# Kernel optimization log

Measured on AMD Instinct MI355X. Metric: run time of the kernel, lower is better.

The kernel has to match this reference:

```python
import jax, jax.numpy as jnp
import numpy as np

# module config
D = 1024      # d_model
H = 16        # n_heads
DK = D // H   # head dim (rotary dim)
HI = 4        # indexer heads
DI = 64       # indexer dim
K = 512       # layer_top_k (adaptive_k fixed to layer default)
B, S = 2, 2048


def setup_inputs() -> dict:
    key = jax.random.key(0)
    ks = jax.random.split(key, 6)
    sc = 0.02
    return {
        "x": jax.random.normal(ks[0], (B, S, D), jnp.float32),
        "w_qkv": jax.random.normal(ks[1], (3 * D, D), jnp.float32) * sc,
        "w_o": jax.random.normal(ks[2], (D, D), jnp.float32) * sc,
        "w_qi": jax.random.normal(ks[3], (HI * DI, D), jnp.float32) * sc,
        "w_ki": jax.random.normal(ks[4], (DI, D), jnp.float32) * sc,
        "w_wi": jax.random.normal(ks[5], (HI, D), jnp.float32) * sc,
    }


def _rope(x):
    # torchtune-style interleaved RoPE; x: [b, s, h, d]
    d = x.shape[-1]
    s = x.shape[1]
    inv = 1.0 / (10000.0 ** (jnp.arange(0, d, 2, dtype=jnp.float32) / d))
    ang = jnp.arange(s, dtype=jnp.float32)[:, None] * inv  # [s, d/2]
    cos = jnp.cos(ang)[None, :, None, :]
    sin = jnp.sin(ang)[None, :, None, :]
    x1, x2 = x[..., ::2], x[..., 1::2]
    return jnp.stack([x1 * cos - x2 * sin, x1 * sin + x2 * cos], axis=-1).reshape(x.shape)


def reference(x, w_qkv, w_o, w_qi, w_ki, w_wi):
    b, s, _ = x.shape
    # QKV projection -> [b, s, 3, H, DK]
    qkv = (x @ w_qkv.T).reshape(b, s, 3, H, DK)
    q, k, v = qkv[:, :, 0], qkv[:, :, 1], qkv[:, :, 2]  # [b, s, h, dk]
    q = _rope(q)
    k = _rope(k)

    # Lightning indexer: I[t,s] = sum_j w[t,j] * relu(q_idx[t,j] . k_idx[s])
    qi = (x @ w_qi.T).reshape(b, s, HI, DI)
    ki = x @ w_ki.T            # [b, s, DI]
    wi = x @ w_wi.T            # [b, s, HI]
    dots = jnp.einsum('bthd,bsd->bths', qi, ki)
    idx_scores = (jax.nn.relu(dots) * wi[:, :, :, None]).sum(axis=2)  # [b, t, s]

    # causal mask then top-k selection -> boolean allow-mask via scatter
    causal = jnp.triu(jnp.ones((s, s), dtype=bool), 1)
    masked_scores = jnp.where(causal[None], -jnp.inf, idx_scores)
    _, top_idx = jax.lax.top_k(masked_scores, K)  # [b, t, K]
    allow = jnp.zeros((b, s, s), dtype=bool).at[
        jnp.arange(b)[:, None, None], jnp.arange(s)[None, :, None], top_idx
    ].set(True)

    # gated sparse attention: SDPA with additive mask (0 where selected, -inf else)
    scores = jnp.einsum('bthd,bshd->bhts', q, k) / jnp.sqrt(jnp.float32(DK))
    scores = jnp.where(allow[:, None], scores, -jnp.inf)
    attn = jax.nn.softmax(scores, axis=-1)
    out = jnp.einsum('bhts,bshd->bthd', attn, v).reshape(b, s, D)
    return out @ w_o.T
```

## Files before the change

### kernel.cpp

```cpp
#include <hip/hip_runtime.h>
#include <hip/hip_bf16.h>
#include <math.h>

namespace {

constexpr int cB = 2, cS = 2048, cD = 1024, cH = 16, cHI = 4, cDI = 64, cK = 512;
constexpr int cNT = cB * cS;
constexpr int QKV_STRIDE = 3 * cD;

typedef __bf16 bf16x8 __attribute__((ext_vector_type(8)));
typedef float f32x4 __attribute__((ext_vector_type(4)));

__device__ __forceinline__ unsigned packbf2(float a, float b)
{
    __hip_bfloat16 ba = __float2bfloat16(a), bb = __float2bfloat16(b);
    return (unsigned)*(unsigned short*)&ba | ((unsigned)*(unsigned short*)&bb << 16);
}

__global__ void pack_bf16(const float* __restrict__ src, __hip_bfloat16* __restrict__ dst, int n)
{
    int i = blockIdx.x * 256 + threadIdx.x;
    if (i < n) dst[i] = __float2bfloat16(src[i]);
}

__global__ __launch_bounds__(256) void mfma_gemm_bt(const __hip_bfloat16* __restrict__ A,
                                                    const __hip_bfloat16* __restrict__ B,
                                                    float* __restrict__ C, int M, int N, int K)
{
    __shared__ unsigned short Als[128][40];
    __shared__ unsigned short Bls[128][40];
    const int tid = threadIdx.x;
    const int m0 = blockIdx.y * 128, n0 = blockIdx.x * 128;
    const int w = tid >> 6, lane = tid & 63;
    const int mw = (w >> 1) * 64, nw = (w & 1) * 64;
    const int lr = lane & 15, quad = lane >> 4;
    const unsigned short* Au = (const unsigned short*)A;
    const unsigned short* Bu = (const unsigned short*)B;
    f32x4 acc[4][4] = {};
    for (int k0 = 0; k0 < K; k0 += 32) {
#pragma unroll
        for (int i = 0; i < 2; i++) {
            int c = tid + i * 256;
            int row = c >> 2, kc = c & 3;
            uint4 av = *(const uint4*)(Au + (size_t)(m0 + row) * K + k0 + kc * 8);
            uint4 bv = *(const uint4*)(Bu + (size_t)(n0 + row) * K + k0 + kc * 8);
            *(uint4*)&Als[row][kc * 8] = av;
            *(uint4*)&Bls[row][kc * 8] = bv;
        }
        __syncthreads();
        bf16x8 af[4], bfr[4];
#pragma unroll
        for (int i = 0; i < 4; i++) af[i] = *(const bf16x8*)&Als[mw + i * 16 + lr][quad * 8];
#pragma unroll
        for (int j = 0; j < 4; j++) bfr[j] = *(const bf16x8*)&Bls[nw + j * 16 + lr][quad * 8];
#pragma unroll
        for (int i = 0; i < 4; i++)
#pragma unroll
            for (int j = 0; j < 4; j++)
                acc[i][j] = __builtin_amdgcn_mfma_f32_16x16x32_bf16(af[i], bfr[j], acc[i][j], 0, 0, 0);
        __syncthreads();
    }
#pragma unroll
    for (int i = 0; i < 4; i++)
#pragma unroll
        for (int j = 0; j < 4; j++)
#pragma unroll
            for (int r = 0; r < 4; r++) {
                int m = m0 + mw + i * 16 + quad * 4 + r;
                int n = n0 + nw + j * 16 + lr;
                C[(size_t)m * N + n] = acc[i][j][r];
            }
}

__global__ void gemm_idx(const float* __restrict__ A, const float* __restrict__ w_qi,
                         const float* __restrict__ w_ki, const float* __restrict__ w_wi,
                         float* __restrict__ qi, float* __restrict__ ki, float* __restrict__ wi)
{
    __shared__ float As[32][68];
    __shared__ float Bs[32][68];
    const int tid = threadIdx.x;
    const int m0 = blockIdx.y * 64, n0 = blockIdx.x * 64;
    const int ty = tid >> 4, tx = tid & 15;
    float acc[4][4] = {};
    for (int k0 = 0; k0 < cD; k0 += 32) {
#pragma unroll
        for (int i = 0; i < 8; i++) {
            int idx = tid + i * 256;
            int r = idx >> 5, kk = idx & 31;
            As[kk][r] = A[(size_t)(m0 + r) * cD + k0 + kk];
            const int nr = n0 + r;
            float bv = 0.f;
            if (nr < 256) bv = w_qi[(size_t)nr * cD + k0 + kk];
            else if (nr < 320) bv = w_ki[(size_t)(nr - 256) * cD + k0 + kk];
            else if (nr < 324) bv = w_wi[(size_t)(nr - 320) * cD + k0 + kk];
            Bs[kk][r] = bv;
        }
        __syncthreads();
#pragma unroll
        for (int kk = 0; kk < 32; kk++) {
            float a[4], b[4];
#pragma unroll
            for (int i = 0; i < 4; i++) a[i] = As[kk][ty * 4 + i];
#pragma unroll
            for (int j = 0; j < 4; j++) b[j] = Bs[kk][tx * 4 + j];
#pragma unroll
            for (int i = 0; i < 4; i++)
#pragma unroll
                for (int j = 0; j < 4; j++) acc[i][j] = fmaf(a[i], b[j], acc[i][j]);
        }
        __syncthreads();
    }
#pragma unroll
    for (int i = 0; i < 4; i++) {
        int m = m0 + ty * 4 + i;
#pragma unroll
        for (int j = 0; j < 4; j++) {
            int n = n0 + tx * 4 + j;
            if (n < 256) qi[(size_t)m * 256 + n] = acc[i][j];
            else if (n < 320) ki[(size_t)m * 64 + (n - 256)] = acc[i][j];
            else if (n < 324) wi[(size_t)m * 4 + (n - 320)] = acc[i][j];
        }
    }
}

__global__ void rope_pack(const float* __restrict__ qkv, __hip_bfloat16* __restrict__ qkvb)
{
    const int idx = blockIdx.x * 256 + threadIdx.x;
    const int c = idx & 511, tok = idx >> 9;
    const int i = c & 31;
    const int s = tok & (cS - 1);
    const float inv = powf(10000.f, -(float)(2 * i) / 64.f);
    float sn, cs;
    sincosf((float)s * inv, &sn, &cs);
    const size_t base = (size_t)tok * QKV_STRIDE + (c >> 5) * 64 + 2 * i;
    unsigned* dst = (unsigned*)qkvb;
    float x1 = qkv[base], x2 = qkv[base + 1];
    dst[base >> 1] = packbf2(x1 * cs - x2 * sn, x1 * sn + x2 * cs);
    x1 = qkv[base + cD]; x2 = qkv[base + cD + 1];
    dst[(base + cD) >> 1] = packbf2(x1 * cs - x2 * sn, x1 * sn + x2 * cs);
    dst[(base + 2 * cD) >> 1] = packbf2(qkv[base + 2 * cD], qkv[base + 2 * cD + 1]);
}

__global__ __launch_bounds__(256) void indexer_scores(const float* __restrict__ qi,
                                                      const float* __restrict__ ki,
                                                      const float* __restrict__ wi,
                                                      float* __restrict__ scores)
{
    const int b = blockIdx.z;
    const int t0 = blockIdx.y * 128, s0 = blockIdx.x * 64;
    if (s0 > t0 + 127) return;
    __shared__ float Qs[128][68];
    __shared__ float Ks[64][68];
    const int tid = threadIdx.x;
    const int ty = tid >> 4, tx = tid & 15;
#pragma unroll
    for (int i = 0; i < 4; i++) {
        int c = tid + i * 256;
        int r = c >> 4, cq = c & 15;
        *(float4*)&Ks[r][cq * 4] = *(const float4*)&ki[((size_t)(b * cS + s0 + r)) * cDI + cq * 4];
    }
    float acc[8][4] = {};
    for (int h = 0; h < cHI; h++) {
        __syncthreads();
#pragma unroll
        for (int i = 0; i < 8; i++) {
            int c = tid + i * 256;
            int r = c >> 4, cq = c & 15;
            *(float4*)&Qs[r][cq * 4] =
                *(const float4*)&qi[((size_t)(b * cS + t0 + r)) * (cHI * cDI) + h * cDI + cq * 4];
        }
        __syncthreads();
        float w8[8];
#pragma unroll
        for (int i = 0; i < 8; i++) w8[i] = wi[((size_t)(b * cS + t0 + ty + i * 16)) * cHI + h];
        float dot[8][4] = {};
        for (int d = 0; d < 64; d += 4) {
            float4 a4[8], b4[4];
#pragma unroll
            for (int i = 0; i < 8; i++) a4[i] = *(const float4*)&Qs[ty + i * 16][d];
#pragma unroll
            for (int j = 0; j < 4; j++) b4[j] = *(const float4*)&Ks[tx + j * 16][d];
#pragma unroll
            for (int i = 0; i < 8; i++)
#pragma unroll
                for (int j = 0; j < 4; j++) {
                    dot[i][j] = fmaf(a4[i].x, b4[j].x, dot[i][j]);
                    dot[i][j] = fmaf(a4[i].y, b4[j].y, dot[i][j]);
                    dot[i][j] = fmaf(a4[i].z, b4[j].z, dot[i][j]);
                    dot[i][j] = fmaf(a4[i].w, b4[j].w, dot[i][j]);
                }
        }
#pragma unroll
        for (int i = 0; i < 8; i++)
#pragma unroll
            for (int j = 0; j < 4; j++) acc[i][j] += fmaxf(dot[i][j], 0.f) * w8[i];
    }
#pragma unroll
    for (int i = 0; i < 8; i++) {
        int t = t0 + ty + i * 16;
#pragma unroll
        for (int j = 0; j < 4; j++) {
            int s = s0 + tx + j * 16;
            if (s <= t) scores[((size_t)(b * cS) + t) * cS + s] = acc[i][j];
        }
    }
}

__device__ __forceinline__ unsigned mapf(float f)
{
    unsigned u = __float_as_uint(f);
    if (u == 0x80000000u) u = 0u;
    return (u & 0x80000000u) ? ~u : (u | 0x80000000u);
}

__global__ void topk_select(const float* __restrict__ scores, unsigned* __restrict__ allow_w)
{
    const int row = blockIdx.x;
    const int t = row & (cS - 1);
    const int tid = threadIdx.x;
    unsigned* aw = allow_w + (size_t)row * 64;
    if (t < cK) {
        if (tid < 64) aw[tid] = (tid < 16) ? 0xFFFFFFFFu : 0u;
        return;
    }
    const float* sr = scores + (size_t)row * cS;
    const int n = t + 1;
    __shared__ unsigned ukeys[cS];
    __shared__ int whist[4][16];
    __shared__ unsigned abits[64];
    __shared__ int wsum[4];
    __shared__ unsigned sh_prefix;
    __shared__ int sh_rem, sh_eqbase;
    for (int s = tid; s < n; s += 256) ukeys[s] = mapf(sr[s]);
    if (tid < 64) abits[tid] = 0u;
    if (tid == 0) { sh_prefix = 0u; sh_rem = cK; }
    __syncthreads();
    const int wl = tid >> 6, ln = tid & 63;
    for (int pass = 0; pass < 8; pass++) {
        const int shift = 28 - 4 * pass;
        const unsigned prefix = sh_prefix;
        const unsigned himask = pass ? (0xFFFFFFFFu << (shift + 4)) : 0u;
        unsigned cnt = 0;
        for (int sb = wl * 64; sb < n; sb += 256) {
            const int s = sb + ln;
            const bool active = (s < n) && ((ukeys[s] & himask) == prefix);
            const unsigned digit = active ? ((ukeys[s] >> shift) & 15u) : 0xFFu;
#pragma unroll
            for (int bin = 0; bin < 16; bin++) {
                const unsigned long long bal = __ballot(active && (digit == (unsigned)bin));
                if (ln == bin) cnt += (unsigned)__popcll(bal);
            }
        }
        if (ln < 16) whist[wl][ln] = (int)cnt;
        __syncthreads();
        if (tid == 0) {
            int rem = sh_rem, cum = 0, d = 15;
            for (; d > 0; d--) {
                const int hd = whist[0][d] + whist[1][d] + whist[2][d] + whist[3][d];
                if (cum + hd >= rem) break;
                cum += hd;
            }
            sh_prefix = prefix | ((unsigned)d << shift);
            sh_rem = rem - cum;
        }
        __syncthreads();
    }
    const unsigned Tu = sh_prefix;
    const int needEq = sh_rem;
    if (tid == 0) sh_eqbase = 0;
    __syncthreads();
    for (int s0 = 0; s0 < n; s0 += 256) {
        const int s = s0 + tid;
        const bool valid = s < n;
        const unsigned u = valid ? ukeys[s] : 0u;
        const bool gt = valid && (u > Tu);
        const bool eq = valid && (u == Tu);
        const unsigned long long bal = __ballot(eq);
        if (ln == 0) wsum[wl] = __popcll(bal);
        __syncthreads();
        int wpre = 0;
        for (int q = 0; q < wl; q++) wpre += wsum[q];
        const int eq_exc = sh_eqbase + wpre + __popcll(bal & ((1ull << ln) - 1ull));
        if (gt || (eq && eq_exc < needEq))
            atomicOr(&abits[s >> 5], 1u << (s & 31));
        const int eq_tot = wsum[0] + wsum[1] + wsum[2] + wsum[3];
        __syncthreads();
        if (tid == 0) sh_eqbase += eq_tot;
        __syncthreads();
    }
    if (tid < 64) aw[tid] = abits[tid];
}

__global__ __launch_bounds__(256) void flash_attn(const __hip_bfloat16* __restrict__ qkvb,
                                                  const unsigned* __restrict__ allow_w,
                                                  __hip_bfloat16* __restrict__ ao)
{
    __shared__ unsigned short Kls[64][76];
    __shared__ unsigned short Vt[64][74];
    __shared__ unsigned short Pls[4][16][74];
    __shared__ uint2 mask_l[64];
    const int ttile = 31 - blockIdx.x;
    const int h = blockIdx.y;
    const int b = blockIdx.z;
    const int tid = threadIdx.x;
    const int w = tid >> 6, lane = tid & 63;
    const int lr = lane & 15, quad = lane >> 4;
    const int tok0 = b * cS + ttile * 64;
    const unsigned short* qkvu = (const unsigned short*)qkvb;

    bf16x8 aq[2];
    {
        const size_t qoff = (size_t)(tok0 + w * 16 + lr) * QKV_STRIDE + h * 64 + quad * 8;
        aq[0] = *(const bf16x8*)(qkvu + qoff);
        aq[1] = *(const bf16x8*)(qkvu + qoff + 32);
    }

    f32x4 O[4] = {};
    float m_r[4], l_r[4];
#pragma unroll
    for (int r = 0; r < 4; r++) { m_r[r] = -INFINITY; l_r[r] = 0.f; }

    const int ktmax = (ttile > 7) ? ttile : 7;
    for (int kt = 0; kt <= ktmax; kt++) {
#pragma unroll
        for (int i = 0; i < 2; i++) {
            const int idx = tid + i * 256;
            const int key = idx >> 3, dg = idx & 7;
            const size_t base = (size_t)(b * cS + kt * 64 + key) * QKV_STRIDE + h * 64 + dg * 8;
            uint4 kv = *(const uint4*)(qkvu + cD + base);
            *(uint4*)&Kls[key][dg * 8] = kv;
            uint4 vv = *(const uint4*)(qkvu + 2 * cD + base);
            const unsigned short* vs = (const unsigned short*)&vv;
#pragma unroll
            for (int jj = 0; jj < 8; jj++) Vt[dg * 8 + jj][key] = vs[jj];
        }
        if (tid < 64) mask_l[tid] = *(const uint2*)&allow_w[(size_t)(tok0 + tid) * 64 + kt * 2];
        __syncthreads();

        f32x4 S[4];
#pragma unroll
        for (int j = 0; j < 4; j++) {
            bf16x8 bk0 = *(const bf16x8*)&Kls[j * 16 + lr][quad * 8];
            bf16x8 bk1 = *(const bf16x8*)&Kls[j * 16 + lr][32 + quad * 8];
            f32x4 s = {};
            s = __builtin_amdgcn_mfma_f32_16x16x32_bf16(aq[0], bk0, s, 0, 0, 0);
            s = __builtin_amdgcn_mfma_f32_16x16x32_bf16(aq[1], bk1, s, 0, 0, 0);
            S[j] = s;
        }

        uint2 mrow[4];
#pragma unroll
        for (int r = 0; r < 4; r++) mrow[r] = mask_l[w * 16 + quad * 4 + r];
#pragma unroll
        for (int j = 0; j < 4; j++) {
            const int sh = (j & 1) * 16 + lr;
#pragma unroll
            for (int r = 0; r < 4; r++) {
                const unsigned mw = (j < 2) ? mrow[r].x : mrow[r].y;
                S[j][r] = ((mw >> sh) & 1u) ? S[j][r] * 0.125f : -INFINITY;
            }
        }

        float alpha[4], mu[4];
#pragma unroll
        for (int r = 0; r < 4; r++) {
            float tm = fmaxf(fmaxf(S[0][r], S[1][r]), fmaxf(S[2][r], S[3][r]));
#pragma unroll
            for (int msk = 8; msk; msk >>= 1) tm = fmaxf(tm, __shfl_xor(tm, msk));
            const float mnew = fmaxf(m_r[r], tm);
            const float mu_old = fmaxf(m_r[r], -1e30f);
            mu[r] = fmaxf(mnew, -1e30f);
            alpha[r] = __expf(mu_old - mu[r]);
            m_r[r] = mnew;
        }
        float rs[4] = {};
#pragma unroll
        for (int j = 0; j < 4; j++) {
#pragma unroll
            for (int r = 0; r < 4; r++) {
                const float p = __expf(S[j][r] - mu[r]);
                rs[r] += p;
                const __hip_bfloat16 pb = __float2bfloat16(p);
                Pls[w][quad * 4 + r][j * 16 + lr] = *(const unsigned short*)&pb;
            }
        }
#pragma unroll
        for (int r = 0; r < 4; r++) {
            float s = rs[r];
#pragma unroll
            for (int msk = 8; msk; msk >>= 1) s += __shfl_xor(s, msk);
            l_r[r] = l_r[r] * alpha[r] + s;
#pragma unroll
            for (int j = 0; j < 4; j++) O[j][r] *= alpha[r];
        }
        __syncthreads();

        bf16x8 ap0 = *(const bf16x8*)&Pls[w][lr][quad * 8];
        bf16x8 ap1 = *(const bf16x8*)&Pls[w][lr][32 + quad * 8];
#pragma unroll
        for (int j = 0; j < 4; j++) {
            bf16x8 bv0 = *(const bf16x8*)&Vt[j * 16 + lr][quad * 8];
            bf16x8 bv1 = *(const bf16x8*)&Vt[j * 16 + lr][32 + quad * 8];
            O[j] = __builtin_amdgcn_mfma_f32_16x16x32_bf16(ap0, bv0, O[j], 0, 0, 0);
            O[j] = __builtin_amdgcn_mfma_f32_16x16x32_bf16(ap1, bv1, O[j], 0, 0, 0);
        }
        __syncthreads();
    }

#pragma unroll
    for (int r = 0; r < 4; r++) {
        const float linv = 1.f / l_r[r];
        const size_t orow = (size_t)(tok0 + w * 16 + quad * 4 + r) * cD + h * 64;
#pragma unroll
        for (int j = 0; j < 4; j++)
            ao[orow + j * 16 + lr] = __float2bfloat16(O[j][r] * linv);
    }
}

}

extern "C" void kernel_launch(void* const* d_in, const int* in_sizes, int n_in,
                              void* d_out, int out_size, void* d_ws, size_t ws_size,
                              hipStream_t stream)
{
    const float* x     = (const float*)d_in[0];
    const float* w_qkv = (const float*)d_in[1];
    const float* w_o   = (const float*)d_in[2];
    const float* w_qi  = (const float*)d_in[3];
    const float* w_ki  = (const float*)d_in[4];
    const float* w_wi  = (const float*)d_in[5];
    float* out = (float*)d_out;

    float* qkv    = (float*)d_ws;
    float* qi     = qkv + (size_t)cNT * QKV_STRIDE;
    float* ki     = qi + (size_t)cNT * cHI * cDI;
    float* wi     = ki + (size_t)cNT * cDI;
    float* scores = wi + (size_t)cNT * cHI;
    unsigned* allow_w = (unsigned*)(scores + (size_t)cB * cS * cS);
    __hip_bfloat16* wo_bf = (__hip_bfloat16*)(allow_w + (size_t)cNT * 64);

    __hip_bfloat16* x_bf    = (__hip_bfloat16*)scores;
    __hip_bfloat16* wqkv_bf = x_bf + (size_t)cNT * cD;
    __hip_bfloat16* ao_bf  = (__hip_bfloat16*)scores;
    __hip_bfloat16* qkv_bf = ao_bf + (size_t)cNT * cD;

    pack_bf16<<<cNT * cD / 256, 256, 0, stream>>>(x, x_bf, cNT * cD);
    pack_bf16<<<3 * cD * cD / 256, 256, 0, stream>>>(w_qkv, wqkv_bf, 3 * cD * cD);
    mfma_gemm_bt<<<dim3(3 * cD / 128, cNT / 128), 256, 0, stream>>>(x_bf, wqkv_bf, qkv, cNT, 3 * cD, cD);
    gemm_idx<<<dim3(6, cNT / 64), 256, 0, stream>>>(x, w_qi, w_ki, w_wi, qi, ki, wi);
    indexer_scores<<<dim3(cS / 64, cS / 128, cB), 256, 0, stream>>>(qi, ki, wi, scores);
    topk_select<<<cNT, 256, 0, stream>>>(scores, allow_w);
    rope_pack<<<cNT * 512 / 256, 256, 0, stream>>>(qkv, qkv_bf);
    pack_bf16<<<cD * cD / 256, 256, 0, stream>>>(w_o, wo_bf, cD * cD);
    flash_attn<<<dim3(cS / 64, cH, cB), 256, 0, stream>>>(qkv_bf, allow_w, ao_bf);
    mfma_gemm_bt<<<dim3(cD / 128, cNT / 128), 256, 0, stream>>>(ao_bf, wo_bf, out, cNT, cD, cD);
}
```

Measured before the change: 626.2 us.

## Double-buffer indexer GEMM and flash attention, skip empty key tiles, bit-sliced histogram

Gives the fp32 indexer GEMM register-staged double buffering so global loads of the next k-slice overlap FMA work. Replaces the 16-ballot-per-bin radix histogram in top-k with five ballots and bitwise masking. Adds a union_mask kernel that records which 64-key tiles have any selected key for each 64-query tile, so flash attention skips key tiles that are fully masked. Flash attention is also double-buffered across K, V and mask tiles. The cost is more LDS, more registers, and one extra small kernel launch.

```diff
diff --git a/kernel.cpp b/kernel.cpp
--- a/kernel.cpp
+++ b/kernel.cpp
@@ -72,43 +72,61 @@
             }
 }
 
-__global__ void gemm_idx(const float* __restrict__ A, const float* __restrict__ w_qi,
-                         const float* __restrict__ w_ki, const float* __restrict__ w_wi,
-                         float* __restrict__ qi, float* __restrict__ ki, float* __restrict__ wi)
-{
-    __shared__ float As[32][68];
-    __shared__ float Bs[32][68];
+__global__ __launch_bounds__(256) void gemm_idx(const float* __restrict__ A, const float* __restrict__ w_qi,
+                                                const float* __restrict__ w_ki, const float* __restrict__ w_wi,
+                                                float* __restrict__ qi, float* __restrict__ ki, float* __restrict__ wi)
+{
+    __shared__ float As[2][32][68];
+    __shared__ float Bs[2][32][68];
     const int tid = threadIdx.x;
     const int m0 = blockIdx.y * 64, n0 = blockIdx.x * 64;
     const int ty = tid >> 4, tx = tid & 15;
-    float acc[4][4] = {};
-    for (int k0 = 0; k0 < cD; k0 += 32) {
+    const int r = tid >> 5, kk = tid & 31;
+    float aR[8], bR[8];
+
+    auto loadStage = [&](int k0) {
 #pragma unroll
         for (int i = 0; i < 8; i++) {
-            int idx = tid + i * 256;
-            int r = idx >> 5, kk = idx & 31;
-            As[kk][r] = A[(size_t)(m0 + r) * cD + k0 + kk];
-            const int nr = n0 + r;
+            aR[i] = A[(size_t)(m0 + r + i * 8) * cD + k0 + kk];
+            const int nr = n0 + r + i * 8;
             float bv = 0.f;
             if (nr < 256) bv = w_qi[(size_t)nr * cD + k0 + kk];
             else if (nr < 320) bv = w_ki[(size_t)(nr - 256) * cD + k0 + kk];
             else if (nr < 324) bv = w_wi[(size_t)(nr - 320) * cD + k0 + kk];
-            Bs[kk][r] = bv;
-        }
-        __syncthreads();
-#pragma unroll
-        for (int kk = 0; kk < 32; kk++) {
+            bR[i] = bv;
+        }
+    };
+    auto commitStage = [&](int bf) {
+#pragma unroll
+        for (int i = 0; i < 8; i++) {
+            As[bf][kk][r + i * 8] = aR[i];
+            Bs[bf][kk][r + i * 8] = bR[i];
+        }
+    };
+
+    loadStage(0);
+    commitStage(0);
+    __syncthreads();
+    float acc[4][4] = {};
+    for (int s = 0; s < 32; s++) {
+        const int cb = s & 1;
+        if (s < 31) loadStage((s + 1) * 32);
+#pragma unroll
+        for (int kx = 0; kx < 32; kx++) {
             float a[4], b[4];
 #pragma unroll
-            for (int i = 0; i < 4; i++) a[i] = As[kk][ty * 4 + i];
-#pragma unroll
-            for (int j = 0; j < 4; j++) b[j] = Bs[kk][tx * 4 + j];
+            for (int i = 0; i < 4; i++) a[i] = As[cb][kx][ty * 4 + i];
+#pragma unroll
+            for (int j = 0; j < 4; j++) b[j] = Bs[cb][kx][tx * 4 + j];
 #pragma unroll
             for (int i = 0; i < 4; i++)
 #pragma unroll
                 for (int j = 0; j < 4; j++) acc[i][j] = fmaf(a[i], b[j], acc[i][j]);
         }
-        __syncthreads();
+        if (s < 31) {
+            commitStage(cb ^ 1);
+            __syncthreads();
+        }
     }
 #pragma unroll
     for (int i = 0; i < 4; i++) {
@@ -244,11 +262,19 @@
         for (int sb = wl * 64; sb < n; sb += 256) {
             const int s = sb + ln;
             const bool active = (s < n) && ((ukeys[s] & himask) == prefix);
-            const unsigned digit = active ? ((ukeys[s] >> shift) & 15u) : 0xFFu;
-#pragma unroll
-            for (int bin = 0; bin < 16; bin++) {
-                const unsigned long long bal = __ballot(active && (digit == (unsigned)bin));
-                if (ln == bin) cnt += (unsigned)__popcll(bal);
+            const unsigned d = active ? ((ukeys[s] >> shift) & 15u) : 0u;
+            const unsigned long long bA = __ballot(active);
+            const unsigned long long b0 = __ballot((d & 1u) != 0u);
+            const unsigned long long b1 = __ballot((d & 2u) != 0u);
+            const unsigned long long b2 = __ballot((d & 4u) != 0u);
+            const unsigned long long b3 = __ballot((d & 8u) != 0u);
+            if (ln < 16) {
+                unsigned long long mres = bA;
+                mres &= (ln & 1) ? b0 : ~b0;
+                mres &= (ln & 2) ? b1 : ~b1;
+                mres &= (ln & 4) ? b2 : ~b2;
+                mres &= (ln & 8) ? b3 : ~b3;
+                cnt += (unsigned)__popcll(mres);
             }
         }
         if (ln < 16) whist[wl][ln] = (int)cnt;
@@ -291,14 +317,31 @@
     if (tid < 64) aw[tid] = abits[tid];
 }
 
+__global__ void union_mask(const unsigned* __restrict__ allow_w, unsigned* __restrict__ umask_any)
+{
+    const int bt = blockIdx.x;
+    const int wd = threadIdx.x;
+    const unsigned* base = allow_w + (size_t)bt * 64 * 64 + wd;
+    unsigned u = 0;
+    for (int rr = 0; rr < 64; rr++) u |= base[rr * 64];
+    const unsigned long long bal = __ballot(u != 0u);
+    if (wd == 0) {
+        unsigned any = 0;
+        for (int kt = 0; kt < 32; kt++)
+            if ((bal >> (2 * kt)) & 3ull) any |= 1u << kt;
+        umask_any[bt] = any;
+    }
+}
+
 __global__ __launch_bounds__(256) void flash_attn(const __hip_bfloat16* __restrict__ qkvb,
                                                   const unsigned* __restrict__ allow_w,
+                                                  const unsigned* __restrict__ umask_any,
                                                   __hip_bfloat16* __restrict__ ao)
 {
-    __shared__ unsigned short Kls[64][76];
-    __shared__ unsigned short Vt[64][74];
+    __shared__ unsigned short Kls[2][64][76];
+    __shared__ unsigned short Vt[2][64][74];
     __shared__ unsigned short Pls[4][16][74];
-    __shared__ uint2 mask_l[64];
+    __shared__ uint2 mask_l[2][64];
     const int ttile = 31 - blockIdx.x;
     const int h = blockIdx.y;
     const int b = blockIdx.z;
@@ -321,36 +364,57 @@
     for (int r = 0; r < 4; r++) { m_r[r] = -INFINITY; l_r[r] = 0.f; }
 
     const int ktmax = (ttile > 7) ? ttile : 7;
-    for (int kt = 0; kt <= ktmax; kt++) {
+    unsigned todo = umask_any[b * 32 + ttile];
+    todo &= (ktmax == 31) ? 0xFFFFFFFFu : ((1u << (ktmax + 1)) - 1u);
+
+    uint4 kreg[2], vreg[2];
+    uint2 mreg = {0u, 0u};
+    auto issue = [&](int kt) {
 #pragma unroll
         for (int i = 0; i < 2; i++) {
             const int idx = tid + i * 256;
             const int key = idx >> 3, dg = idx & 7;
             const size_t base = (size_t)(b * cS + kt * 64 + key) * QKV_STRIDE + h * 64 + dg * 8;
-            uint4 kv = *(const uint4*)(qkvu + cD + base);
-            *(uint4*)&Kls[key][dg * 8] = kv;
-            uint4 vv = *(const uint4*)(qkvu + 2 * cD + base);
-            const unsigned short* vs = (const unsigned short*)&vv;
-#pragma unroll
-            for (int jj = 0; jj < 8; jj++) Vt[dg * 8 + jj][key] = vs[jj];
-        }
-        if (tid < 64) mask_l[tid] = *(const uint2*)&allow_w[(size_t)(tok0 + tid) * 64 + kt * 2];
-        __syncthreads();
+            kreg[i] = *(const uint4*)(qkvu + cD + base);
+            vreg[i] = *(const uint4*)(qkvu + 2 * cD + base);
+        }
+        if (tid < 64) mreg = *(const uint2*)&allow_w[(size_t)(tok0 + tid) * 64 + kt * 2];
+    };
+    auto commit = [&](int bf) {
+#pragma unroll
+        for (int i = 0; i < 2; i++) {
+            const int idx = tid + i * 256;
+            const int key = idx >> 3, dg = idx & 7;
+            *(uint4*)&Kls[bf][key][dg * 8] = kreg[i];
+            const unsigned short* vs = (const unsigned short*)&vreg[i];
+#pragma unroll
+            for (int jj = 0; jj < 8; jj++) Vt[bf][dg * 8 + jj][key] = vs[jj];
+        }
+        if (tid < 64) mask_l[bf][tid] = mreg;
+    };
+
+    issue(__ffs(todo) - 1);
+    todo &= todo - 1;
+    commit(0);
+    __syncthreads();
+    int buf = 0;
+    for (;;) {
+        const int ktn = todo ? (__ffs(todo) - 1) : -1;
+        if (ktn >= 0) { todo &= todo - 1; issue(ktn); }
 
         f32x4 S[4];
 #pragma unroll
         for (int j = 0; j < 4; j++) {
-            bf16x8 bk0 = *(const bf16x8*)&Kls[j * 16 + lr][quad * 8];
-            bf16x8 bk1 = *(const bf16x8*)&Kls[j * 16 + lr][32 + quad * 8];
+            bf16x8 bk0 = *(const bf16x8*)&Kls[buf][j * 16 + lr][quad * 8];
+            bf16x8 bk1 = *(const bf16x8*)&Kls[buf][j * 16 + lr][32 + quad * 8];
             f32x4 s = {};
             s = __builtin_amdgcn_mfma_f32_16x16x32_bf16(aq[0], bk0, s, 0, 0, 0);
             s = __builtin_amdgcn_mfma_f32_16x16x32_bf16(aq[1], bk1, s, 0, 0, 0);
             S[j] = s;
         }
-
         uint2 mrow[4];
 #pragma unroll
-        for (int r = 0; r < 4; r++) mrow[r] = mask_l[w * 16 + quad * 4 + r];
+        for (int r = 0; r < 4; r++) mrow[r] = mask_l[buf][w * 16 + quad * 4 + r];
 #pragma unroll
         for (int j = 0; j < 4; j++) {
             const int sh = (j & 1) * 16 + lr;
@@ -360,7 +424,6 @@
                 S[j][r] = ((mw >> sh) & 1u) ? S[j][r] * 0.125f : -INFINITY;
             }
         }
-
         float alpha[4], mu[4];
 #pragma unroll
         for (int r = 0; r < 4; r++) {
@@ -399,12 +462,15 @@
         bf16x8 ap1 = *(const bf16x8*)&Pls[w][lr][32 + quad * 8];
 #pragma unroll
         for (int j = 0; j < 4; j++) {
-            bf16x8 bv0 = *(const bf16x8*)&Vt[j * 16 + lr][quad * 8];
-            bf16x8 bv1 = *(const bf16x8*)&Vt[j * 16 + lr][32 + quad * 8];
+            bf16x8 bv0 = *(const bf16x8*)&Vt[buf][j * 16 + lr][quad * 8];
+            bf16x8 bv1 = *(const bf16x8*)&Vt[buf][j * 16 + lr][32 + quad * 8];
             O[j] = __builtin_amdgcn_mfma_f32_16x16x32_bf16(ap0, bv0, O[j], 0, 0, 0);
             O[j] = __builtin_amdgcn_mfma_f32_16x16x32_bf16(ap1, bv1, O[j], 0, 0, 0);
         }
-        __syncthreads();
+        if (ktn < 0) break;
+        commit(buf ^ 1);
+        __syncthreads();
+        buf ^= 1;
     }
 
 #pragma unroll
@@ -436,8 +502,9 @@
     float* ki     = qi + (size_t)cNT * cHI * cDI;
     float* wi     = ki + (size_t)cNT * cDI;
     float* scores = wi + (size_t)cNT * cHI;
-    unsigned* allow_w = (unsigned*)(scores + (size_t)cB * cS * cS);
+    unsigned* allow_w   = (unsigned*)(scores + (size_t)cB * cS * cS);
     __hip_bfloat16* wo_bf = (__hip_bfloat16*)(allow_w + (size_t)cNT * 64);
+    unsigned* umask_any = (unsigned*)(wo_bf + (size_t)cD * cD);
 
     __hip_bfloat16* x_bf    = (__hip_bfloat16*)scores;
     __hip_bfloat16* wqkv_bf = x_bf + (size_t)cNT * cD;
@@ -450,8 +517,9 @@
     gemm_idx<<<dim3(6, cNT / 64), 256, 0, stream>>>(x, w_qi, w_ki, w_wi, qi, ki, wi);
     indexer_scores<<<dim3(cS / 64, cS / 128, cB), 256, 0, stream>>>(qi, ki, wi, scores);
     topk_select<<<cNT, 256, 0, stream>>>(scores, allow_w);
+    union_mask<<<cB * 32, 64, 0, stream>>>(allow_w, umask_any);
     rope_pack<<<cNT * 512 / 256, 256, 0, stream>>>(qkv, qkv_bf);
     pack_bf16<<<cD * cD / 256, 256, 0, stream>>>(w_o, wo_bf, cD * cD);
-    flash_attn<<<dim3(cS / 64, cH, cB), 256, 0, stream>>>(qkv_bf, allow_w, ao_bf);
+    flash_attn<<<dim3(cS / 64, cH, cB), 256, 0, stream>>>(qkv_bf, allow_w, umask_any, ao_bf);
     mfma_gemm_bt<<<dim3(cD / 128, cNT / 128), 256, 0, stream>>>(ao_bf, wo_bf, out, cNT, cD, cD);
 }
```

Result: faster. 604.5 us (-3.5%).
